# Kernel optimization log

Measured on AMD Instinct MI355X. Metric: run time of the kernel, lower is better.

Reference implementation:

```python
import jax, jax.numpy as jnp
import numpy as np

DIM = 2048
HEAD_DIM = 64
NUM_HEADS = DIM // HEAD_DIM
ROT_DIM = HEAD_DIM // 2  # 32
THETA = 10000.0
LN_EPS = 1e-5


def setup_inputs() -> dict:
    key = jax.random.key(0)
    ks = jax.random.split(key, 6)
    n, s = 2, 2048
    x = jax.random.normal(ks[0], (n, s, DIM), dtype=jnp.float32)
    ln_w = jnp.ones((DIM,), dtype=jnp.float32)
    ln_b = jnp.zeros((DIM,), dtype=jnp.float32)
    # Linear weights stored as (in, out); torch Linear init scale ~ 1/sqrt(in)
    sc = 1.0 / np.sqrt(DIM)
    w_qkv = jax.random.uniform(ks[1], (DIM, 3 * DIM), jnp.float32, -sc, sc)
    b_qkv = jax.random.uniform(ks[2], (3 * DIM,), jnp.float32, -sc, sc)
    w_out = jax.random.uniform(ks[3], (DIM, DIM), jnp.float32, -sc, sc)
    b_out = jax.random.uniform(ks[4], (DIM,), jnp.float32, -sc, sc)
    return {"x": x, "ln_w": ln_w, "ln_b": ln_b, "w_qkv": w_qkv,
            "b_qkv": b_qkv, "w_out": w_out, "b_out": b_out}


def _rope_cos_sin(seq_len):
    # freqs: theta ** linspace(0, -1, rot_dim//2 + 1)[:-1] -> 16 freqs
    n_freq = ROT_DIM // 2
    exps = jnp.linspace(0.0, -1.0, n_freq + 1)[:-1]
    freqs = THETA ** exps  # [16]
    pos = jnp.arange(seq_len, dtype=jnp.float32)  # [s]
    tmp = pos[:, None] * freqs[None, :]  # [s, 16]
    # broadcast target: [1, 1, s, 16] over (n, h, s, d)
    return jnp.cos(tmp)[None, None], jnp.sin(tmp)[None, None]


def _apply_rotary(x, cos, sin):
    d = cos.shape[-1]  # 16
    x1, x2, x3 = x[..., :d], x[..., d:2 * d], x[..., 2 * d:]
    y1 = x1 * cos - x2 * sin
    y2 = x2 * cos + x1 * sin
    return jnp.concatenate([y1.astype(x3.dtype), y2.astype(x3.dtype), x3], axis=-1)


def reference(x, ln_w, ln_b, w_qkv, b_qkv, w_out, b_out):
    n, s, dim = x.shape
    skip = x
    # LayerNorm
    mu = jnp.mean(x, axis=-1, keepdims=True)
    var = jnp.var(x, axis=-1, keepdims=True)
    h = (x - mu) * jax.lax.rsqrt(var + LN_EPS) * ln_w + ln_b
    # fused QKV projection
    qkv = h @ w_qkv + b_qkv  # [n, s, 3*dim]
    qkv = qkv.reshape(n, s, 3, NUM_HEADS, HEAD_DIM)
    qkv = jnp.transpose(qkv, (2, 0, 3, 1, 4))  # [3, n, h, s, d]
    q, k, v = qkv[0], qkv[1], qkv[2]
    # RoPE on first rot_dim dims
    cos, sin = _rope_cos_sin(s)
    q = _apply_rotary(q, cos, sin)
    k = _apply_rotary(k, cos, sin)
    # causal SDPA
    scale = 1.0 / jnp.sqrt(jnp.asarray(HEAD_DIM, dtype=q.dtype))
    scores = jnp.einsum('nhqd,nhkd->nhqk', q, k) * scale
    causal = jnp.tril(jnp.ones((s, s), dtype=bool))
    scores = jnp.where(causal[None, None], scores, jnp.asarray(-jnp.inf, scores.dtype))
    attn = jax.nn.softmax(scores, axis=-1)
    o = jnp.einsum('nhqk,nhkd->nhqd', attn, v)  # [n, h, s, d]
    o = jnp.transpose(o, (0, 2, 1, 3)).reshape(n, s, dim)
    return o @ w_out + b_out + skip
```

## Files before the change

kernel.cpp:

```cpp
#include <hip/hip_runtime.h>
#include <hip/hip_bf16.h>
#include <cstdint>
#include <cstddef>

#define DIMM 2048
#define NHEADS 32
#define HDIM 64
#define SEQ 2048
#define NBATCH 2
#define ROWS 4096
#define NFREQ 16
#define NKT3 32
#define QSCALE 0.1803368802f

#define PB_LN ROWS
#define PB_TQKV (192 * 64)
#define PB_TOUT (64 * 64)
#define PB_ROPE ((SEQ * NFREQ + 255) / 256)
#define PB_TOTAL (PB_LN + PB_TQKV + PB_TOUT + PB_ROPE)

typedef __bf16 bfv8 __attribute__((ext_vector_type(8)));
typedef float f32x4v __attribute__((ext_vector_type(4)));
typedef float f32x16 __attribute__((ext_vector_type(16)));

__device__ __forceinline__ void gload16(const void* g, void* l) {
  __builtin_amdgcn_global_load_lds((const __attribute__((address_space(1))) void*)g,
                                   (__attribute__((address_space(3))) void*)l, 16, 0, 0);
}

__device__ __forceinline__ f32x4v mfma16(bfv8 a, bfv8 b, f32x4v c) {
  return __builtin_amdgcn_mfma_f32_16x16x32_bf16(a, b, c, 0, 0, 0);
}

__device__ __forceinline__ f32x16 mfma32(bfv8 a, bfv8 b, f32x16 c) {
  return __builtin_amdgcn_mfma_f32_32x32x16_bf16(a, b, c, 0, 0, 0);
}

__device__ __forceinline__ unsigned short f2bfu(float f) {
  __hip_bfloat16 h = __float2bfloat16(f);
  return __builtin_bit_cast(unsigned short, h);
}

__device__ __forceinline__ void swap32(unsigned& a, unsigned& b, const int hi) {
  const unsigned ta = (unsigned)__shfl_xor((int)a, 32);
  const unsigned tb = (unsigned)__shfl_xor((int)b, 32);
  const unsigned na = hi ? tb : a;
  const unsigned nb = hi ? b : ta;
  a = na;
  b = nb;
}

__device__ __forceinline__ void xcd_swizzle(int& bx, int& by) {
  const int gx = gridDim.x, nwg = gx * gridDim.y;
  const int orig = blockIdx.y * gx + blockIdx.x;
  const int q = nwg >> 3, r = nwg & 7;
  const int xcd = orig & 7, loc = orig >> 3;
  const int wg = (xcd < r ? xcd * (q + 1) : r * (q + 1) + (xcd - r) * q) + loc;
  bx = wg % gx;
  by = wg / gx;
}

__device__ __forceinline__ void transpose32_body(const float* __restrict__ W,
                                                 __hip_bfloat16* __restrict__ WT,
                                                 int K, int N, int n0, int k0,
                                                 float* tile ) {
  const int tid = threadIdx.x;
  const int tx = tid & 31, ty = tid >> 5;
#pragma unroll
  for (int j = 0; j < 4; ++j)
    tile[(ty + j * 8) * 33 + tx] = W[(size_t)(k0 + ty + j * 8) * N + n0 + tx];
  __syncthreads();
#pragma unroll
  for (int j = 0; j < 4; ++j)
    WT[(size_t)(n0 + ty + j * 8) * K + k0 + tx] = __float2bfloat16(tile[tx * 33 + ty + j * 8]);
}

__global__ __launch_bounds__(256) void prep_kernel(
    const float* __restrict__ x, const float* __restrict__ lw, const float* __restrict__ lb,
    __hip_bfloat16* __restrict__ h, const float* __restrict__ w_qkv,
    __hip_bfloat16* __restrict__ wqkvT, const float* __restrict__ w_out,
    __hip_bfloat16* __restrict__ woutT, float* __restrict__ ct, float* __restrict__ st) {
  __shared__ float pls[32 * 33];
  const int b = blockIdx.x;
  const int t = threadIdx.x;
  if (b < PB_LN) {
    const int row = b;
    const float4* xr = (const float4*)(x + (size_t)row * DIMM);
    float4 a = xr[t * 2], bb4 = xr[t * 2 + 1];
    float e[8];
    *(float4*)e = a; *(float4*)(e + 4) = bb4;
    float s = 0.f, ss = 0.f;
#pragma unroll
    for (int j = 0; j < 8; ++j) { s += e[j]; ss += e[j] * e[j]; }
#pragma unroll
    for (int o = 1; o < 64; o <<= 1) { s += __shfl_xor(s, o); ss += __shfl_xor(ss, o); }
    float* red = pls;
    const int wid = t >> 6;
    if ((t & 63) == 0) { red[wid * 2] = s; red[wid * 2 + 1] = ss; }
    __syncthreads();
    s = red[0] + red[2] + red[4] + red[6];
    ss = red[1] + red[3] + red[5] + red[7];
    const float mu = s * (1.f / DIMM);
    const float var = ss * (1.f / DIMM) - mu * mu;
    const float rs = rsqrtf(var + 1e-5f);
    const float4* w4 = (const float4*)lw;
    const float4* b4 = (const float4*)lb;
    float4 wa = w4[t * 2], wb = w4[t * 2 + 1], ba = b4[t * 2], bb = b4[t * 2 + 1];
    float wv[8], bv[8];
    *(float4*)wv = wa; *(float4*)(wv + 4) = wb;
    *(float4*)bv = ba; *(float4*)(bv + 4) = bb;
    unsigned short hv[8];
#pragma unroll
    for (int j = 0; j < 8; ++j)
      hv[j] = f2bfu((e[j] - mu) * rs * wv[j] + bv[j]);
    *(uint4*)((char*)h + (size_t)row * (DIMM * 2) + t * 16) = *(uint4*)hv;
  } else if (b < PB_LN + PB_TQKV) {
    const int i = b - PB_LN;
    const int n0 = (i % 192) * 32, k0 = (i / 192) * 32;
    transpose32_body(w_qkv, wqkvT, DIMM, 3 * DIMM, n0, k0, pls);
  } else if (b < PB_LN + PB_TQKV + PB_TOUT) {
    const int i = b - PB_LN - PB_TQKV;
    const int n0 = (i % 64) * 32, k0 = (i / 64) * 32;
    transpose32_body(w_out, woutT, DIMM, DIMM, n0, k0, pls);
  } else {
    const int i = (b - PB_LN - PB_TQKV - PB_TOUT) * 256 + t;
    if (i < SEQ * NFREQ) {
      const int pos = i >> 4, f = i & 15;
      const float freq = powf(10000.0f, -(float)f / 16.0f);
      const float ang = (float)pos * freq;
      ct[i] = cosf(ang);
      st[i] = sinf(ang);
    }
  }
}

__device__ __forceinline__ void stageA64(const char* Ab, int brow, int kt,
                                         char* bufA, int c, int lane) {
  const int row = c * 8 + (lane >> 3);
  const int src = ((lane & 7) * 16) ^ ((row & 7) << 4);
  gload16(Ab + (size_t)(brow + row) * 4096 + kt * 128 + src, bufA + c * 1024);
}
__device__ __forceinline__ void stageB64(const char* Bb, int bcol, int kt,
                                         char* bufB, int c, int lane) {
  const int row = c * 8 + (lane >> 3);
  const int src = ((lane & 7) * 16) ^ ((row & 7) << 4);
  gload16(Bb + (size_t)(bcol + row) * 4096 + kt * 128 + src, bufB + c * 1024);
}

__device__ __forceinline__ void gemm_core3(const char* Ab, const char* Bb,
                                           int brow, int bcol, char* lds,
                                           f32x4v acc[8][4]) {
  const int tid = threadIdx.x, lane = tid & 63, wid = tid >> 6;
  const int g = lane >> 4, ln15 = lane & 15;
  const int wr = wid >> 2, wc = (wid >> 1) & 1, wk = wid & 1;
  const int kb = wk * 64;
#pragma unroll
  for (int t = 0; t < 2; ++t) {
    char* bufA = lds + t * 49152;
    char* bufB = bufA + 32768;
    stageA64(Ab, brow, t, bufA, wid, lane);
    stageA64(Ab, brow, t, bufA, wid + 8, lane);
    stageA64(Ab, brow, t, bufA, wid + 16, lane);
    stageA64(Ab, brow, t, bufA, wid + 24, lane);
    stageB64(Bb, bcol, t, bufB, wid, lane);
    stageB64(Bb, bcol, t, bufB, wid + 8, lane);
  }
  asm volatile("s_waitcnt vmcnt(6)" ::: "memory");
  __builtin_amdgcn_s_barrier();

  for (int t = 0; t < NKT3; ++t) {
    char* bufA = lds + (t % 3) * 49152;
    char* bufB = bufA + 32768;
    char* nbufA = lds + ((t + 2) % 3) * 49152;
    char* nbufB = nbufA + 32768;
    const bool st = (t + 2 < NKT3);
    bfv8 af[4], bfr[4];
#pragma unroll
    for (int mi = 0; mi < 4; ++mi) {
      const int ra = wr * 128 + mi * 16 + ln15;
      af[mi] = *(const bfv8*)(bufA + (size_t)ra * 128 + ((kb + g * 16) ^ ((ra & 7) << 4)));
    }
#pragma unroll
    for (int nf = 0; nf < 4; ++nf) {
      const int rb = wc * 64 + nf * 16 + ln15;
      bfr[nf] = *(const bfv8*)(bufB + (size_t)rb * 128 + ((kb + g * 16) ^ ((rb & 7) << 4)));
    }
    if (st) {
      stageA64(Ab, brow, t + 2, nbufA, wid, lane);
      stageA64(Ab, brow, t + 2, nbufA, wid + 8, lane);
      stageB64(Bb, bcol, t + 2, nbufB, wid, lane);
    }
    __builtin_amdgcn_s_setprio(1);
#pragma unroll
    for (int mi = 0; mi < 4; ++mi)
#pragma unroll
      for (int nf = 0; nf < 4; ++nf)
        acc[mi][nf] = mfma16(af[mi], bfr[nf], acc[mi][nf]);
    __builtin_amdgcn_s_setprio(0);
    bfv8 ao[4];
#pragma unroll
    for (int mi = 0; mi < 4; ++mi) {
      const int ra = wr * 128 + (4 + mi) * 16 + ln15;
      ao[mi] = *(const bfv8*)(bufA + (size_t)ra * 128 + ((kb + g * 16) ^ ((ra & 7) << 4)));
    }
    if (st) {
      stageA64(Ab, brow, t + 2, nbufA, wid + 16, lane);
      stageA64(Ab, brow, t + 2, nbufA, wid + 24, lane);
      stageB64(Bb, bcol, t + 2, nbufB, wid + 8, lane);
    }
    __builtin_amdgcn_s_setprio(1);
#pragma unroll
    for (int mi = 0; mi < 4; ++mi)
#pragma unroll
      for (int nf = 0; nf < 4; ++nf)
        acc[4 + mi][nf] = mfma16(ao[mi], bfr[nf], acc[4 + mi][nf]);
    __builtin_amdgcn_s_setprio(0);
    if (st) {
      asm volatile("s_waitcnt vmcnt(6)" ::: "memory");
    } else if (t == NKT3 - 2) {
      asm volatile("s_waitcnt vmcnt(0)" ::: "memory");
    }
    asm volatile("" ::: "memory");
    __builtin_amdgcn_s_barrier();
  }
}

__device__ __forceinline__ void kreduce(char* lds, f32x4v acc[8][4], f32x4v ak[4][4],
                                        int wid, int lane, int wk) {
  char* reg = lds + (size_t)wid * 16384;
#pragma unroll
  for (int q = 0; q < 4; ++q)
#pragma unroll
    for (int nf = 0; nf < 4; ++nf)
      *(f32x4v*)(reg + (q * 4 + nf) * 1024 + lane * 16) = acc[wk ? q : 4 + q][nf];
  __syncthreads();
  const char* preg = lds + (size_t)(wid ^ 1) * 16384;
#pragma unroll
  for (int q = 0; q < 4; ++q)
#pragma unroll
    for (int nf = 0; nf < 4; ++nf)
      ak[q][nf] = acc[wk ? 4 + q : q][nf] +
                  *(const f32x4v*)(preg + (q * 4 + nf) * 1024 + lane * 16);
  __syncthreads();
}

__global__ __launch_bounds__(512, 2) void gemm_qkv_kernel(
    const __hip_bfloat16* __restrict__ A, const __hip_bfloat16* __restrict__ BT,
    const float* __restrict__ bqkv, const float* __restrict__ ct, const float* __restrict__ st,
    __hip_bfloat16* __restrict__ qb, __hip_bfloat16* __restrict__ kb,
    __hip_bfloat16* __restrict__ vb) {
  __shared__ char lds[147456];
  const f32x4v fz = {0.f, 0.f, 0.f, 0.f};
  f32x4v acc[8][4];
#pragma unroll
  for (int mf = 0; mf < 8; ++mf)
#pragma unroll
    for (int nf = 0; nf < 4; ++nf) acc[mf][nf] = fz;
  int bx, by;
  xcd_swizzle(bx, by);
  const int brow = by * 256, bcol = bx * 128;
  gemm_core3((const char*)A, (const char*)BT, brow, bcol, lds, acc);

  const int tid = threadIdx.x, lane = tid & 63, wid = tid >> 6;
  const int g = lane >> 4, ln15 = lane & 15;
  const int wr = wid >> 2, wc = (wid >> 1) & 1, wk = wid & 1;
  f32x4v ak[4][4];
  kreduce(lds, acc, ak, wid, lane, wk);

  const int cb = bcol + wc * 64;
  const int which = cb >> 11;
  const int head = (cb & 2047) >> 6;
  const int rowbase = brow + wr * 128 + wk * 64;
  const int nidx = rowbase >> 11;
  const int posb = rowbase & 2047;
  float bias[4];
#pragma unroll
  for (int nf = 0; nf < 4; ++nf) bias[nf] = bqkv[cb + nf * 16 + ln15];

  if (which == 2) {
    char* tp = lds + wid * 8192;
    const size_t vhead = ((size_t)nidx * NHEADS + head) * (HDIM * SEQ);
#pragma unroll
    for (int q = 0; q < 4; ++q)
#pragma unroll
      for (int r = 0; r < 4; ++r) {
        const int posl = q * 16 + g * 4 + r;
#pragma unroll
        for (int nf = 0; nf < 4; ++nf) {
          const int d = nf * 16 + ln15;
          *(unsigned short*)(tp + d * 128 + ((posl * 2) ^ ((d & 7) << 4))) =
              f2bfu(ak[q][nf][r] + bias[nf]);
        }
      }
    asm volatile("s_waitcnt lgkmcnt(0)" ::: "memory");
    __builtin_amdgcn_sched_barrier(0);
#pragma unroll
    for (int i = 0; i < 8; ++i) {
      const int dl = i * 8 + (lane >> 3);
      const int cs = (lane & 7) ^ (dl & 7);
      const uint4 val = *(const uint4*)(tp + dl * 128 + cs * 16);
      *(uint4*)((char*)vb + (vhead + (size_t)dl * SEQ + posb + (lane & 7) * 8) * 2) = val;
    }
  } else {
    __hip_bfloat16* dst = (which == 0) ? qb : kb;
    const float qs = (which == 0) ? QSCALE : 1.0f;
    char* tp = lds + wid * 8192;
#pragma unroll
    for (int q = 0; q < 4; ++q)
#pragma unroll
      for (int r = 0; r < 4; ++r) {
        const int posl = q * 16 + g * 4 + r;
        const int pos = posb + posl;
        float v0 = ak[q][0][r] + bias[0];
        float v1 = ak[q][1][r] + bias[1];
        float v2 = ak[q][2][r] + bias[2];
        float v3 = ak[q][3][r] + bias[3];
        const float c0 = ct[pos * 16 + ln15], s0 = st[pos * 16 + ln15];
        const float x1 = v0, x2 = v1;
        v0 = (x1 * c0 - x2 * s0) * qs;
        v1 = (x2 * c0 + x1 * s0) * qs;
        v2 *= qs;
        v3 *= qs;
        const int sw2 = (posl & 7) << 4;
        char* rowp = tp + posl * 128;
        *(unsigned short*)(rowp + ((ln15 * 2) ^ sw2)) = f2bfu(v0);
        *(unsigned short*)(rowp + ((32 + ln15 * 2) ^ sw2)) = f2bfu(v1);
        *(unsigned short*)(rowp + ((64 + ln15 * 2) ^ sw2)) = f2bfu(v2);
        *(unsigned short*)(rowp + ((96 + ln15 * 2) ^ sw2)) = f2bfu(v3);
      }
    asm volatile("s_waitcnt lgkmcnt(0)" ::: "memory");
    __builtin_amdgcn_sched_barrier(0);
    const size_t qkbase = (((size_t)(nidx * NHEADS + head)) * SEQ + posb) * HDIM;
#pragma unroll
    for (int i = 0; i < 8; ++i) {
      const int rr = i * 8 + (lane >> 3);
      const int cs = (lane & 7) ^ (rr & 7);
      const uint4 val = *(const uint4*)(tp + rr * 128 + cs * 16);
      *(uint4*)((char*)dst + (qkbase + (size_t)rr * HDIM) * 2 + (lane & 7) * 16) = val;
    }
  }
}

__global__ __launch_bounds__(512, 2) void gemm_out_kernel(
    const __hip_bfloat16* __restrict__ A, const __hip_bfloat16* __restrict__ BT,
    const float* __restrict__ bout, const float* __restrict__ skip,
    float* __restrict__ out) {
  __shared__ char lds[147456];
  const f32x4v fz = {0.f, 0.f, 0.f, 0.f};
  f32x4v acc[8][4];
#pragma unroll
  for (int mf = 0; mf < 8; ++mf)
#pragma unroll
    for (int nf = 0; nf < 4; ++nf) acc[mf][nf] = fz;
  int bx, by;
  xcd_swizzle(bx, by);
  const int brow = by * 256, bcol = bx * 128;
  gemm_core3((const char*)A, (const char*)BT, brow, bcol, lds, acc);

  const int tid = threadIdx.x, lane = tid & 63, wid = tid >> 6;
  const int g = lane >> 4, ln15 = lane & 15;
  const int wr = wid >> 2, wc = (wid >> 1) & 1, wk = wid & 1;
  f32x4v ak[4][4];
  kreduce(lds, acc, ak, wid, lane, wk);

  const int rowbase = brow + wr * 128 + wk * 64;
  char* tp = lds + wid * 16384;
#pragma unroll
  for (int q = 0; q < 4; ++q)
#pragma unroll
    for (int r = 0; r < 4; ++r) {
      const int posl = q * 16 + g * 4 + r;
      const int sw2 = ((posl >> 2) & 3) << 6;
      char* rowp = tp + posl * 256;
#pragma unroll
      for (int nf = 0; nf < 4; ++nf)
        *(float*)(rowp + ((nf * 64 + ln15 * 4) ^ sw2)) = ak[q][nf][r];
    }
  asm volatile("s_waitcnt lgkmcnt(0)" ::: "memory");
  __builtin_amdgcn_sched_barrier(0);
  const int colb = bcol + wc * 64;
#pragma unroll
  for (int i = 0; i < 16; ++i) {
    const int rr = i * 4 + (lane >> 4);
    const int cp = lane & 15;
    const float4 a4 = *(const float4*)(tp + rr * 256 + cp * 16);
    const int lc = (cp * 16) ^ (((rr >> 2) & 3) << 6);
    const int col = colb + (lc >> 2);
    const int row = rowbase + rr;
    const float4 sk = *(const float4*)(skip + (size_t)row * DIMM + col);
    const float4 bo = *(const float4*)(bout + col);
    float4 o4;
    o4.x = a4.x + sk.x + bo.x;
    o4.y = a4.y + sk.y + bo.y;
    o4.z = a4.z + sk.z + bo.z;
    o4.w = a4.w + sk.w + bo.w;
    *(float4*)(out + (size_t)row * DIMM + col) = o4;
  }
}

__global__ __launch_bounds__(256) void attn_kernel(
    const __hip_bfloat16* __restrict__ qb, const __hip_bfloat16* __restrict__ kb,
    const __hip_bfloat16* __restrict__ vtb, __hip_bfloat16* __restrict__ ob) {
  __shared__ char sm[49664];
  float* lred = (float*)(sm + 49152);
  const int tid = threadIdx.x, lane = tid & 63, wid = tid >> 6;
  const int ln31 = lane & 31, hi = lane >> 5;
  const int head = blockIdx.x;
  const int qbi = (int)gridDim.y - 1 - (int)blockIdx.y;
  const size_t hb = (size_t)head * (SEQ * HDIM);
  const int q0 = qbi * 128;
  const int qw = q0 + wid * 32;
  const int qg = qw + ln31;
  const int nt = qbi * 2 + 2;
  const char* Kg = (const char*)(kb + hb);
  const char* Vg = (const char*)(vtb + hb);

  bfv8 qf[4];
  {
    const char* Qp = (const char*)(qb + hb) + (size_t)(qw + ln31) * 128 + hi * 16;
#pragma unroll
    for (int j = 0; j < 4; ++j) qf[j] = *(const bfv8*)(Qp + j * 32);
  }

  f32x16 o0, o1;
#pragma unroll
  for (int i = 0; i < 16; ++i) { o0[i] = 0.f; o1[i] = 0.f; }
  float m_run = -1e30f, l_run = 0.f;
  const int swz = (ln31 & 7) << 4;

#define ATTN_STAGE(T, B)                                                            \
  {                                                                                 \
    const int kvs = (T)*64;                                                         \
    _Pragma("unroll") for (int i = 0; i < 2; ++i) {                                 \
      const int f = (tid + i * 256) * 16;                                           \
      const int row = f >> 7;                                                       \
      const int src = (f & 127) ^ ((row & 7) << 4);                                 \
      gload16(Kg + (size_t)(kvs + row) * 128 + src, sm + (B)*8192 + f);             \
      gload16(Vg + (size_t)row * 4096 + (size_t)kvs * 2 + src,                      \
              sm + 24576 + (B)*8192 + f);                                           \
    }                                                                               \
  }

  ATTN_STAGE(0, 0);
  if (nt > 1) ATTN_STAGE(1, 1);
  asm volatile("s_waitcnt vmcnt(4)" ::: "memory");
  __builtin_amdgcn_s_barrier();

  for (int t = 0; t < nt; ++t) {
    const int kvb = t * 64;
    const bool st = (t + 2 < nt);
    if (st) ATTN_STAGE(t + 2, (t + 2) % 3);
    if (kvb <= qw + 31) {
      const char* ldsK = sm + (t % 3) * 8192;
      const char* ldsV = sm + 24576 + (t % 3) * 8192;
      f32x16 s0, s1;
#pragma unroll
      for (int i = 0; i < 16; ++i) { s0[i] = 0.f; s1[i] = 0.f; }
      __builtin_amdgcn_s_setprio(1);
#pragma unroll
      for (int j = 0; j < 4; ++j) {
        const int byt = j * 32 + hi * 16;
        const bfv8 k0 = *(const bfv8*)(ldsK + ln31 * 128 + (byt ^ swz));
        const bfv8 k1 = *(const bfv8*)(ldsK + (32 + ln31) * 128 + (byt ^ swz));
        s0 = mfma32(k0, qf[j], s0);
        s1 = mfma32(k1, qf[j], s1);
      }
      __builtin_amdgcn_s_setprio(0);
      float p[32];
#pragma unroll
      for (int r = 0; r < 16; ++r) { p[r] = s0[r]; p[16 + r] = s1[r]; }
      if (kvb + 63 > qw) {
#pragma unroll
        for (int r = 0; r < 16; ++r) {
          const int kvo = (r & 3) + 8 * (r >> 2) + 4 * hi;
          if (kvb + kvo > qg) p[r] = -1e30f;
          if (kvb + 32 + kvo > qg) p[16 + r] = -1e30f;
        }
      }
      float mx = p[0];
#pragma unroll
      for (int r = 1; r < 32; ++r) mx = fmaxf(mx, p[r]);
      mx = fmaxf(mx, __shfl_xor(mx, 32));
      if (!__all(mx <= m_run + 8.0f)) {
        const float mn = fmaxf(m_run, mx);
        const float al = __builtin_amdgcn_exp2f(m_run - mn);
        m_run = mn;
        l_run *= al;
        lred[wid * 32 + ln31] = al;
        asm volatile("s_waitcnt lgkmcnt(0)" ::: "memory");
        __builtin_amdgcn_sched_barrier(0);
#pragma unroll
        for (int r = 0; r < 16; ++r) {
          const float a = lred[wid * 32 + (r & 3) + 8 * (r >> 2) + 4 * hi];
          o0[r] *= a;
          o1[r] *= a;
        }
      }
      float ps = 0.f;
#pragma unroll
      for (int r = 0; r < 32; ++r) {
        p[r] = __builtin_amdgcn_exp2f(p[r] - m_run);
        ps += p[r];
      }
      ps += __shfl_xor(ps, 32);
      l_run += ps;
      unsigned c[16];
#pragma unroll
      for (int i = 0; i < 16; ++i) {
        unsigned rr;
        asm("v_cvt_pk_bf16_f32 %0, %1, %2" : "=v"(rr) : "v"(p[2 * i]), "v"(p[2 * i + 1]));
        c[i] = rr;
      }
      bfv8 paf[4];
#pragma unroll
      for (int fI = 0; fI < 4; ++fI) {
        unsigned a0 = c[fI * 4 + 0], b0 = c[fI * 4 + 2];
        unsigned a1 = c[fI * 4 + 1], b1 = c[fI * 4 + 3];
        swap32(a0, b0, hi);
        swap32(a1, b1, hi);
        union { unsigned u[4]; bfv8 v; } w;
        w.u[0] = a0; w.u[1] = a1; w.u[2] = b0; w.u[3] = b1;
        paf[fI] = w.v;
      }
      __builtin_amdgcn_s_setprio(1);
#pragma unroll
      for (int ss = 0; ss < 4; ++ss) {
        const int byt = ss * 32 + hi * 16;
        const bfv8 v0 = *(const bfv8*)(ldsV + ln31 * 128 + (byt ^ swz));
        const bfv8 v1 = *(const bfv8*)(ldsV + (32 + ln31) * 128 + (byt ^ swz));
        o0 = mfma32(paf[ss], v0, o0);
        o1 = mfma32(paf[ss], v1, o1);
      }
      __builtin_amdgcn_s_setprio(0);
    }
    if (st) {
      asm volatile("s_waitcnt vmcnt(4)" ::: "memory");
    } else if (t + 1 < nt) {
      asm volatile("s_waitcnt vmcnt(0)" ::: "memory");
    }
    asm volatile("" ::: "memory");
    __builtin_amdgcn_s_barrier();
  }
#undef ATTN_STAGE

  lred[wid * 32 + ln31] = l_run;
  asm volatile("s_waitcnt lgkmcnt(0)" ::: "memory");
  __builtin_amdgcn_sched_barrier(0);
  const int nidx = head >> 5, hh = head & 31;
#pragma unroll
  for (int r = 0; r < 16; ++r) {
    const int qrow = qw + (r & 3) + 8 * (r >> 2) + 4 * hi;
    const float inv = 1.0f / lred[wid * 32 + (r & 3) + 8 * (r >> 2) + 4 * hi];
    __hip_bfloat16* dst = ob + ((size_t)nidx * SEQ + qrow) * DIMM + hh * 64;
    dst[ln31] = __float2bfloat16(o0[r] * inv);
    dst[32 + ln31] = __float2bfloat16(o1[r] * inv);
  }
}

extern "C" void kernel_launch(void* const* d_in, const int* in_sizes, int n_in,
                              void* d_out, int out_size, void* d_ws, size_t ws_size,
                              hipStream_t stream) {
  const float* x = (const float*)d_in[0];
  const float* ln_w = (const float*)d_in[1];
  const float* ln_b = (const float*)d_in[2];
  const float* w_qkv = (const float*)d_in[3];
  const float* b_qkv = (const float*)d_in[4];
  const float* w_out = (const float*)d_in[5];
  const float* b_out = (const float*)d_in[6];
  float* out = (float*)d_out;

  char* ws = (char*)d_ws;
  size_t off = 0;
  auto alloc = [&](size_t bytes) -> char* {
    char* p = ws + off;
    off += (bytes + 255) & ~(size_t)255;
    return p;
  };
  __hip_bfloat16* h = (__hip_bfloat16*)alloc((size_t)ROWS * DIMM * 2);
  __hip_bfloat16* wqkvT = (__hip_bfloat16*)alloc((size_t)3 * DIMM * DIMM * 2);
  __hip_bfloat16* woutT = (__hip_bfloat16*)alloc((size_t)DIMM * DIMM * 2);
  __hip_bfloat16* qbuf = (__hip_bfloat16*)alloc((size_t)ROWS * DIMM * 2);
  __hip_bfloat16* kbuf = (__hip_bfloat16*)alloc((size_t)ROWS * DIMM * 2);
  __hip_bfloat16* vtbuf = (__hip_bfloat16*)alloc((size_t)ROWS * DIMM * 2);
  __hip_bfloat16* obuf = (__hip_bfloat16*)alloc((size_t)ROWS * DIMM * 2);
  float* ct = (float*)alloc((size_t)SEQ * NFREQ * 4);
  float* st = (float*)alloc((size_t)SEQ * NFREQ * 4);

  prep_kernel<<<dim3(PB_TOTAL), dim3(256), 0, stream>>>(
      x, ln_w, ln_b, h, w_qkv, wqkvT, w_out, woutT, ct, st);
  gemm_qkv_kernel<<<dim3(3 * DIMM / 128, ROWS / 256), dim3(512), 0, stream>>>(
      h, wqkvT, b_qkv, ct, st, qbuf, kbuf, vtbuf);
  attn_kernel<<<dim3(NBATCH * NHEADS, SEQ / 128), dim3(256), 0, stream>>>(
      qbuf, kbuf, vtbuf, obuf);
  gemm_out_kernel<<<dim3(DIMM / 128, ROWS / 256), dim3(512), 0, stream>>>(
      obuf, woutT, b_out, x, out);
}
```

Baseline: 254.7 us.

## Software-pipeline attention loop so next-tile QK MFMAs overlap current softmax/PV

The attention inner loop is restructured into a two-tile unrolled pipeline. The QK^T MFMA for tile t+1 is issued before the softmax and PV of tile t, and two score accumulators alternate between tiles. The aim is to hide the exp and reduction latency of the softmax behind matrix-core work. In exchange it holds 32 more fp32 accumulator registers, which may hurt occupancy. It also tightens the global-load waits to vmcnt(0), which reduces how far the prefetch can run ahead.

```diff
diff --git a/kernel.cpp b/kernel.cpp
--- a/kernel.cpp
+++ b/kernel.cpp
@@ -441,104 +441,116 @@
     }                                                                               \
   }
 
+  auto qk_tile = [&](int b, f32x16& d0, f32x16& d1) {
+    const char* ldsK = sm + b * 8192;
+    f32x16 a0, a1;
+#pragma unroll
+    for (int i = 0; i < 16; ++i) { a0[i] = 0.f; a1[i] = 0.f; }
+    __builtin_amdgcn_s_setprio(1);
+#pragma unroll
+    for (int j = 0; j < 4; ++j) {
+      const int byt = j * 32 + hi * 16;
+      const bfv8 k0 = *(const bfv8*)(ldsK + ln31 * 128 + (byt ^ swz));
+      const bfv8 k1 = *(const bfv8*)(ldsK + (32 + ln31) * 128 + (byt ^ swz));
+      a0 = mfma32(k0, qf[j], a0);
+      a1 = mfma32(k1, qf[j], a1);
+    }
+    __builtin_amdgcn_s_setprio(0);
+    d0 = a0;
+    d1 = a1;
+  };
+
+  auto sm_pv = [&](f32x16& s0, f32x16& s1, int kvb, int b) {
+    const char* ldsV = sm + 24576 + b * 8192;
+    if (kvb + 63 > qw) {
+#pragma unroll
+      for (int r = 0; r < 16; ++r) {
+        const int kvo = (r & 3) + 8 * (r >> 2) + 4 * hi;
+        if (kvb + kvo > qg) s0[r] = -1e30f;
+        if (kvb + 32 + kvo > qg) s1[r] = -1e30f;
+      }
+    }
+    float m8[8];
+#pragma unroll
+    for (int r = 0; r < 8; ++r)
+      m8[r] = fmaxf(fmaxf(s0[r], s0[8 + r]), fmaxf(s1[r], s1[8 + r]));
+    float m4a = fmaxf(m8[0], m8[4]), m4b = fmaxf(m8[1], m8[5]);
+    float m4c = fmaxf(m8[2], m8[6]), m4d = fmaxf(m8[3], m8[7]);
+    float mx = fmaxf(fmaxf(m4a, m4b), fmaxf(m4c, m4d));
+    mx = fmaxf(mx, __shfl_xor(mx, 32));
+    if (!__all(mx <= m_run + 8.0f)) {
+      const float mn = fmaxf(m_run, mx);
+      const float al = __builtin_amdgcn_exp2f(m_run - mn);
+      m_run = mn;
+      l_run *= al;
+      lred[wid * 32 + ln31] = al;
+      asm volatile("s_waitcnt lgkmcnt(0)" ::: "memory");
+      __builtin_amdgcn_sched_barrier(0);
+#pragma unroll
+      for (int r = 0; r < 16; ++r) {
+        const float a = lred[wid * 32 + (r & 3) + 8 * (r >> 2) + 4 * hi];
+        o0[r] *= a;
+        o1[r] *= a;
+      }
+    }
+    float ps = 0.f;
+#pragma unroll
+    for (int r = 0; r < 16; ++r) {
+      s0[r] = __builtin_amdgcn_exp2f(s0[r] - m_run);
+      s1[r] = __builtin_amdgcn_exp2f(s1[r] - m_run);
+      ps += s0[r] + s1[r];
+    }
+    ps += __shfl_xor(ps, 32);
+    l_run += ps;
+    unsigned c[16];
+#pragma unroll
+    for (int i = 0; i < 8; ++i) {
+      unsigned r0, r1;
+      asm("v_cvt_pk_bf16_f32 %0, %1, %2" : "=v"(r0) : "v"(s0[2 * i]), "v"(s0[2 * i + 1]));
+      asm("v_cvt_pk_bf16_f32 %0, %1, %2" : "=v"(r1) : "v"(s1[2 * i]), "v"(s1[2 * i + 1]));
+      c[i] = r0;
+      c[8 + i] = r1;
+    }
+    bfv8 paf[4];
+#pragma unroll
+    for (int fI = 0; fI < 4; ++fI) {
+      unsigned a0 = c[fI * 4 + 0], b0 = c[fI * 4 + 2];
+      unsigned a1 = c[fI * 4 + 1], b1 = c[fI * 4 + 3];
+      swap32(a0, b0, hi);
+      swap32(a1, b1, hi);
+      union { unsigned u[4]; bfv8 v; } w;
+      w.u[0] = a0; w.u[1] = a1; w.u[2] = b0; w.u[3] = b1;
+      paf[fI] = w.v;
+    }
+    __builtin_amdgcn_s_setprio(1);
+#pragma unroll
+    for (int ss = 0; ss < 4; ++ss) {
+      const int byt = ss * 32 + hi * 16;
+      const bfv8 v0 = *(const bfv8*)(ldsV + ln31 * 128 + (byt ^ swz));
+      const bfv8 v1 = *(const bfv8*)(ldsV + (32 + ln31) * 128 + (byt ^ swz));
+      o0 = mfma32(paf[ss], v0, o0);
+      o1 = mfma32(paf[ss], v1, o1);
+    }
+    __builtin_amdgcn_s_setprio(0);
+  };
+
   ATTN_STAGE(0, 0);
   if (nt > 1) ATTN_STAGE(1, 1);
-  asm volatile("s_waitcnt vmcnt(4)" ::: "memory");
+  asm volatile("s_waitcnt vmcnt(0)" ::: "memory");
   __builtin_amdgcn_s_barrier();
-
-  for (int t = 0; t < nt; ++t) {
-    const int kvb = t * 64;
-    const bool st = (t + 2 < nt);
-    if (st) ATTN_STAGE(t + 2, (t + 2) % 3);
-    if (kvb <= qw + 31) {
-      const char* ldsK = sm + (t % 3) * 8192;
-      const char* ldsV = sm + 24576 + (t % 3) * 8192;
-      f32x16 s0, s1;
-#pragma unroll
-      for (int i = 0; i < 16; ++i) { s0[i] = 0.f; s1[i] = 0.f; }
-      __builtin_amdgcn_s_setprio(1);
-#pragma unroll
-      for (int j = 0; j < 4; ++j) {
-        const int byt = j * 32 + hi * 16;
-        const bfv8 k0 = *(const bfv8*)(ldsK + ln31 * 128 + (byt ^ swz));
-        const bfv8 k1 = *(const bfv8*)(ldsK + (32 + ln31) * 128 + (byt ^ swz));
-        s0 = mfma32(k0, qf[j], s0);
-        s1 = mfma32(k1, qf[j], s1);
-      }
-      __builtin_amdgcn_s_setprio(0);
-      float p[32];
-#pragma unroll
-      for (int r = 0; r < 16; ++r) { p[r] = s0[r]; p[16 + r] = s1[r]; }
-      if (kvb + 63 > qw) {
-#pragma unroll
-        for (int r = 0; r < 16; ++r) {
-          const int kvo = (r & 3) + 8 * (r >> 2) + 4 * hi;
-          if (kvb + kvo > qg) p[r] = -1e30f;
-          if (kvb + 32 + kvo > qg) p[16 + r] = -1e30f;
-        }
-      }
-      float mx = p[0];
-#pragma unroll
-      for (int r = 1; r < 32; ++r) mx = fmaxf(mx, p[r]);
-      mx = fmaxf(mx, __shfl_xor(mx, 32));
-      if (!__all(mx <= m_run + 8.0f)) {
-        const float mn = fmaxf(m_run, mx);
-        const float al = __builtin_amdgcn_exp2f(m_run - mn);
-        m_run = mn;
-        l_run *= al;
-        lred[wid * 32 + ln31] = al;
-        asm volatile("s_waitcnt lgkmcnt(0)" ::: "memory");
-        __builtin_amdgcn_sched_barrier(0);
-#pragma unroll
-        for (int r = 0; r < 16; ++r) {
-          const float a = lred[wid * 32 + (r & 3) + 8 * (r >> 2) + 4 * hi];
-          o0[r] *= a;
-          o1[r] *= a;
-        }
-      }
-      float ps = 0.f;
-#pragma unroll
-      for (int r = 0; r < 32; ++r) {
-        p[r] = __builtin_amdgcn_exp2f(p[r] - m_run);
-        ps += p[r];
-      }
-      ps += __shfl_xor(ps, 32);
-      l_run += ps;
-      unsigned c[16];
-#pragma unroll
-      for (int i = 0; i < 16; ++i) {
-        unsigned rr;
-        asm("v_cvt_pk_bf16_f32 %0, %1, %2" : "=v"(rr) : "v"(p[2 * i]), "v"(p[2 * i + 1]));
-        c[i] = rr;
-      }
-      bfv8 paf[4];
-#pragma unroll
-      for (int fI = 0; fI < 4; ++fI) {
-        unsigned a0 = c[fI * 4 + 0], b0 = c[fI * 4 + 2];
-        unsigned a1 = c[fI * 4 + 1], b1 = c[fI * 4 + 3];
-        swap32(a0, b0, hi);
-        swap32(a1, b1, hi);
-        union { unsigned u[4]; bfv8 v; } w;
-        w.u[0] = a0; w.u[1] = a1; w.u[2] = b0; w.u[3] = b1;
-        paf[fI] = w.v;
-      }
-      __builtin_amdgcn_s_setprio(1);
-#pragma unroll
-      for (int ss = 0; ss < 4; ++ss) {
-        const int byt = ss * 32 + hi * 16;
-        const bfv8 v0 = *(const bfv8*)(ldsV + ln31 * 128 + (byt ^ swz));
-        const bfv8 v1 = *(const bfv8*)(ldsV + (32 + ln31) * 128 + (byt ^ swz));
-        o0 = mfma32(paf[ss], v0, o0);
-        o1 = mfma32(paf[ss], v1, o1);
-      }
-      __builtin_amdgcn_s_setprio(0);
-    }
-    if (st) {
-      asm volatile("s_waitcnt vmcnt(4)" ::: "memory");
-    } else if (t + 1 < nt) {
-      asm volatile("s_waitcnt vmcnt(0)" ::: "memory");
-    }
-    asm volatile("" ::: "memory");
+  f32x16 sA0, sA1, sB0, sB1;
+  qk_tile(0, sA0, sA1);
+
+  for (int t = 0; t < nt; t += 2) {
+    if (t + 2 < nt) ATTN_STAGE(t + 2, (t + 2) % 3);
+    if ((t + 1) * 64 <= qw + 31) qk_tile((t + 1) % 3, sB0, sB1);
+    if (t * 64 <= qw + 31) sm_pv(sA0, sA1, t * 64, t % 3);
+    asm volatile("s_waitcnt vmcnt(0)" ::: "memory");
+    __builtin_amdgcn_s_barrier();
+    if (t + 3 < nt) ATTN_STAGE(t + 3, (t + 3) % 3);
+    if (t + 2 < nt && (t + 2) * 64 <= qw + 31) qk_tile((t + 2) % 3, sA0, sA1);
+    if ((t + 1) * 64 <= qw + 31) sm_pv(sB0, sB1, (t + 1) * 64, (t + 1) % 3);
+    asm volatile("s_waitcnt vmcnt(0)" ::: "memory");
     __builtin_amdgcn_s_barrier();
   }
 #undef ATTN_STAGE
```

After: 294.3 us. +15.5%, slower.
